# Kernel optimization log

Measured on AMD Instinct MI355X. Metric: run time of the kernel, lower is better.

The kernel has to match this reference:

```python
import jax, jax.numpy as jnp
import numpy as np

NODES = 23   # 22 players + ball per frame-graph
K = 8        # random neighbors per node
B, T = 64, 128
G = B * T            # total graphs (frames)
N = G * NODES        # total nodes
D_IN, H, RH = 16, 128, 128


def setup_inputs() -> dict:
    key = jax.random.key(0)
    ks = jax.random.split(key, 10)
    x = jax.random.normal(ks[0], (N, D_IN), jnp.float32)
    # per-graph random edges: dst = each node repeated K times, src = random node in same graph
    src_local = jax.random.randint(ks[1], (G, NODES * K), 0, NODES)
    dst_local = jnp.tile(jnp.repeat(jnp.arange(NODES), K)[None, :], (G, 1))
    off = (jnp.arange(G) * NODES)[:, None]
    edge_index = jnp.stack([(src_local + off).reshape(-1),
                            (dst_local + off).reshape(-1)]).astype(jnp.int32)
    runner_idx = jax.random.randint(ks[2], (G,), 0, NODES, dtype=jnp.int32)
    sc = lambda k, sh: (jax.random.normal(k, sh, jnp.float32) * 0.05)
    return {
        'x': x, 'edge_index': edge_index, 'runner_idx': runner_idx,
        'W1': sc(ks[3], (D_IN, H)), 'b1': jnp.zeros((H,), jnp.float32),
        'W2': sc(ks[4], (H, H)),    'b2': jnp.zeros((H,), jnp.float32),
        'W_ih': sc(ks[5], (3 * RH, H)), 'W_hh': sc(ks[6], (3 * RH, RH)),
        'b_ih': jnp.zeros((3 * RH,), jnp.float32), 'b_hh': jnp.zeros((3 * RH,), jnp.float32),
        'Wp': sc(ks[7], (RH, 2)), 'bp': jnp.zeros((2,), jnp.float32),
    }


def _gcn_conv(h, edge_index, W, b):
    # PyG GCNConv: add self-loops, symmetric normalization, scatter-sum
    h = h @ W
    loop = jnp.arange(N, dtype=edge_index.dtype)
    s = jnp.concatenate([edge_index[0], loop])
    d = jnp.concatenate([edge_index[1], loop])
    deg = jax.ops.segment_sum(jnp.ones_like(s, h.dtype), d, num_segments=N)
    dinv = jnp.where(deg > 0, jax.lax.rsqrt(deg), 0.0)
    norm = dinv[s] * dinv[d]                      # [E+N]
    out = jax.ops.segment_sum(h[s] * norm[:, None], d, num_segments=N)
    return out + b


def _gru(seq, W_ih, W_hh, b_ih, b_hh):
    # torch GRU: gates in r,z,n order
    xg = seq @ W_ih.T + b_ih                      # [B,T,3RH]
    def step(hprev, xt):
        gh = hprev @ W_hh.T + b_hh
        xr, xz, xn = jnp.split(xt, 3, axis=-1)
        hr, hz, hn = jnp.split(gh, 3, axis=-1)
        r = jax.nn.sigmoid(xr + hr)
        z = jax.nn.sigmoid(xz + hz)
        n = jnp.tanh(xn + r * hn)
        hnew = (1.0 - z) * n + z * hprev
        return hnew, hnew
    h0 = jnp.zeros((seq.shape[0], RH), seq.dtype)
    _, outs = jax.lax.scan(step, h0, jnp.swapaxes(xg, 0, 1))
    return jnp.swapaxes(outs, 0, 1)               # [B,T,RH]


def reference(x, edge_index, runner_idx, W1, b1, W2, b2,
              W_ih, W_hh, b_ih, b_hh, Wp, bp):
    h = jax.nn.relu(_gcn_conv(x, edge_index, W1, b1))
    h = jax.nn.relu(_gcn_conv(h, edge_index, W2, b2))
    # fused equivalent of the per-graph nonzero()/indexing loop:
    runner_global = jnp.arange(G, dtype=jnp.int32) * NODES + runner_idx
    seq = h[runner_global].reshape(B, T, H)       # all lengths == T, padding is a no-op
    out = _gru(seq, W_ih, W_hh, b_ih, b_hh)
    return out @ Wp + bp                          # [B,T,2]
```

## Files before the change

### kernel.cpp

```cpp
#include <hip/hip_runtime.h>
#include <hip/hip_bf16.h>
#include <math.h>

#define GG 8192
#define NODESN 23
#define KK 8
#define DIN 16
#define HH 128
#define RHH 128
#define EPG (NODESN*KK)
#define TTT 128
#define BBB 64

__global__ __launch_bounds__(256) void gcn_hsum(
    const float* __restrict__ x, const int* __restrict__ esrc,
    const int* __restrict__ runner,
    const float* __restrict__ W1, const float* __restrict__ b1,
    float* __restrict__ hsum_g)
{
    __shared__ float xs[NODESN * DIN];
    __shared__ int   srcs[EPG];
    __shared__ float t1[NODESN * HH];
    __shared__ float red[256];

    const int g   = blockIdx.x;
    const int tid = threadIdx.x;
    const int j   = tid & 127;
    const int nh  = tid >> 7;

    for (int i = tid; i < NODESN * DIN; i += 256) xs[i] = x[g * NODESN * DIN + i];
    for (int i = tid; i < EPG; i += 256)          srcs[i] = esrc[g * EPG + i] - g * NODESN;

    float w[DIN];
    #pragma unroll
    for (int k = 0; k < DIN; k++) w[k] = W1[k * HH + j];
    const float b1j = b1[j];
    __syncthreads();

    const int n0 = nh * 12;
    const int n1 = nh ? NODESN : 12;
    for (int n = n0; n < n1; n++) {
        float acc = 0.f;
        #pragma unroll
        for (int k = 0; k < DIN; k += 4) {
            float4 xv = *(const float4*)&xs[n * DIN + k];
            acc = fmaf(xv.x, w[k], fmaf(xv.y, w[k+1], fmaf(xv.z, w[k+2], fmaf(xv.w, w[k+3], acc))));
        }
        t1[n * HH + j] = acc;
    }
    __syncthreads();

    const int r = runner[g];
    float part = 0.f;
    for (int slot = nh; slot < 9; slot += 2) {
        int node = (slot < 8) ? srcs[r * KK + slot] : r;
        float acc = t1[node * HH + j];
        #pragma unroll
        for (int k = 0; k < KK; k++) acc += t1[srcs[node * KK + k] * HH + j];
        part += fmaxf(acc * (1.f / 9.f) + b1j, 0.f);
    }
    red[tid] = part;
    __syncthreads();
    if (tid < HH) hsum_g[(size_t)g * HH + tid] = red[tid] + red[tid + 128];
}

__global__ __launch_bounds__(256) void seq_kernel(
    const float* __restrict__ hsum_g, const float* __restrict__ W2,
    const float* __restrict__ b2, float* __restrict__ seq)
{
    __shared__ float hs[16 * HH];
    const int tid = threadIdx.x;
    const int j = tid & 127, mh = tid >> 7;
    const size_t base = (size_t)blockIdx.x * 16 * HH;

    for (int v = tid; v < 16 * HH / 4; v += 256)
        ((float4*)hs)[v] = ((const float4*)(hsum_g + base))[v];
    __syncthreads();

    float acc[8];
    #pragma unroll
    for (int m = 0; m < 8; m++) acc[m] = 0.f;
    const float* hrow = hs + mh * 8 * HH;
    for (int k = 0; k < HH; k += 4) {
        float w0  = W2[(k+0)*HH + j];
        float w1  = W2[(k+1)*HH + j];
        float w2v = W2[(k+2)*HH + j];
        float w3  = W2[(k+3)*HH + j];
        #pragma unroll
        for (int m = 0; m < 8; m++) {
            float4 hv = *(const float4*)&hrow[m * HH + k];
            acc[m] = fmaf(hv.x, w0, fmaf(hv.y, w1, fmaf(hv.z, w2v, fmaf(hv.w, w3, acc[m]))));
        }
    }
    const float bj = b2[j];
    #pragma unroll
    for (int m = 0; m < 8; m++)
        seq[base + (size_t)(mh * 8 + m) * HH + j] = fmaxf(acc[m] * (1.f/9.f) + bj, 0.f);
}

__global__ void transpose_wih(const float* __restrict__ W, float* __restrict__ WT)
{
    int idx = blockIdx.x * 256 + threadIdx.x;
    if (idx < 3 * RHH * RHH) {
        int jj = idx / RHH, kk = idx - jj * RHH;
        WT[kk * (3 * RHH) + jj] = W[idx];
    }
}

__global__ __launch_bounds__(384) void xg_kernel(
    const float* __restrict__ seq, const float* __restrict__ WT,
    const float* __restrict__ b_ih, float* __restrict__ xg)
{
    const int tid = threadIdx.x;
    const int m0 = blockIdx.x * 8;
    const float* srow = seq + (size_t)m0 * RHH;
    float acc[8];
    const float bv = b_ih[tid];
    #pragma unroll
    for (int mi = 0; mi < 8; mi++) acc[mi] = bv;
    for (int k = 0; k < RHH; k += 4) {
        float w0 = WT[(k+0)*384 + tid];
        float w1 = WT[(k+1)*384 + tid];
        float w2 = WT[(k+2)*384 + tid];
        float w3 = WT[(k+3)*384 + tid];
        #pragma unroll
        for (int mi = 0; mi < 8; mi++) {
            float4 sv = *(const float4*)(srow + mi * RHH + k);
            acc[mi] = fmaf(sv.x, w0, fmaf(sv.y, w1, fmaf(sv.z, w2, fmaf(sv.w, w3, acc[mi]))));
        }
    }
    #pragma unroll
    for (int mi = 0; mi < 8; mi++)
        xg[(size_t)(m0 + mi) * 384 + tid] = acc[mi];
}

#define CHUNK 64
#define XGBUF_FLOATS (CHUNK * 3 * RHH)
#define HOUT_FLOATS  (CHUNK * HH)

__global__ __launch_bounds__(1024)
__attribute__((amdgpu_waves_per_eu(4, 4)))
void gru_kernel(
    const float* __restrict__ xg, const float* __restrict__ W_hh,
    const float* __restrict__ b_hh, const float* __restrict__ Wp,
    const float* __restrict__ bp, float* __restrict__ out)
{
    __shared__ float xgbuf[XGBUF_FLOATS];
    __shared__ float houtb[HOUT_FLOATS];
    __shared__ float hpp[2 * HH];
    __shared__ float wps[2 * RHH + 2];

    const int b    = blockIdx.x;
    const int tid  = threadIdx.x;
    const int lane = tid & 63;
    const int q    = lane >> 3;
    const int i    = ((tid >> 6) << 3) | (lane & 7);

    float wr[16], wz[16], wn[16];
    int loff[4];
    {
        const float* br = W_hh + (size_t)i * RHH;
        const float* bz = br + (size_t)RHH * RHH;
        const float* bn = bz + (size_t)RHH * RHH;
        #pragma unroll
        for (int m = 0; m < 4; m++) {
            int p = (m + q) & 3;
            int o = q * 16 + 4 * p;
            loff[m] = o;
            float4 v;
            v = *(const float4*)(br + o); wr[4*m]=v.x; wr[4*m+1]=v.y; wr[4*m+2]=v.z; wr[4*m+3]=v.w;
            v = *(const float4*)(bz + o); wz[4*m]=v.x; wz[4*m+1]=v.y; wz[4*m+2]=v.z; wz[4*m+3]=v.w;
            v = *(const float4*)(bn + o); wn[4*m]=v.x; wn[4*m+1]=v.y; wn[4*m+2]=v.z; wn[4*m+3]=v.w;
        }
    }
    #pragma unroll
    for (int m = 0; m < 16; m++) {
        asm("" : "+v"(wr[m]));
        asm("" : "+v"(wz[m]));
        asm("" : "+v"(wn[m]));
    }

    const float bhr = b_hh[i];
    const float bhz = b_hh[RHH + i];
    const float bhn = b_hh[2 * RHH + i];

    if (tid < 2 * RHH) wps[tid] = Wp[tid];
    if (tid < 2)       wps[2 * RHH + tid] = bp[tid];
    if (tid < HH)      hpp[tid] = 0.f;
    float hprev = 0.f;

    const float* xbase = xg + (size_t)b * TTT * 3 * RHH;
    float* outb = out + (size_t)b * TTT * 2;

    for (int c = 0; c < TTT / CHUNK; c++) {
        {
            const float4* src = (const float4*)(xbase + (size_t)c * XGBUF_FLOATS);
            #pragma unroll
            for (int v = 0; v < XGBUF_FLOATS / 4 / 1024; v++)
                ((float4*)xgbuf)[tid + v * 1024] = src[tid + v * 1024];
        }
        if (c > 0) {
            const int s  = tid & 7;
            const int cc = (tid >> 3) & 1;
            const int tl = tid >> 4;
            const float* hr = &houtb[tl * HH + s * 16];
            float acc = 0.f;
            #pragma unroll
            for (int m = 0; m < 16; m += 4) {
                float4 hv = *(const float4*)(hr + m);
                int k = s * 16 + m;
                acc = fmaf(hv.x, wps[(k+0)*2 + cc],
                      fmaf(hv.y, wps[(k+1)*2 + cc],
                      fmaf(hv.z, wps[(k+2)*2 + cc],
                      fmaf(hv.w, wps[(k+3)*2 + cc], acc))));
            }
            acc += __shfl_xor(acc, 1); acc += __shfl_xor(acc, 2); acc += __shfl_xor(acc, 4);
            if (s == 0)
                outb[((c - 1) * CHUNK + tl) * 2 + cc] = acc + wps[2 * RHH + cc];
        }
        __syncthreads();

        for (int tl = 0; tl < CHUNK; tl++) {
            const float* hrow = &hpp[(tl & 1) * HH];
            float ar = 0.f, az = 0.f, an = 0.f;
            #pragma unroll
            for (int m = 0; m < 4; m++) {
                float4 hv = *(const float4*)(hrow + loff[m]);
                ar = fmaf(hv.x, wr[4*m], fmaf(hv.y, wr[4*m+1], fmaf(hv.z, wr[4*m+2], fmaf(hv.w, wr[4*m+3], ar))));
                az = fmaf(hv.x, wz[4*m], fmaf(hv.y, wz[4*m+1], fmaf(hv.z, wz[4*m+2], fmaf(hv.w, wz[4*m+3], az))));
                an = fmaf(hv.x, wn[4*m], fmaf(hv.y, wn[4*m+1], fmaf(hv.z, wn[4*m+2], fmaf(hv.w, wn[4*m+3], an))));
            }

            ar += __shfl_xor(ar, 8); ar += __shfl_xor(ar, 16); ar += __shfl_xor(ar, 32);
            az += __shfl_xor(az, 8); az += __shfl_xor(az, 16); az += __shfl_xor(az, 32);
            an += __shfl_xor(an, 8); an += __shfl_xor(an, 16); an += __shfl_xor(an, 32);

            {
                float xr = xgbuf[tl * 384 + i];
                float xz = xgbuf[tl * 384 + RHH + i];
                float xn = xgbuf[tl * 384 + 2 * RHH + i];
                float sr = xr + ar + bhr;
                float sz = xz + az + bhz;
                float rg = 1.f / (1.f + __expf(-sr));
                float zg = 1.f / (1.f + __expf(-sz));
                float tv = fmaf(rg, an + bhn, xn);
                tv = fminf(fmaxf(tv, -15.f), 15.f);
                float e2 = __expf(-2.f * tv);
                float ng = (1.f - e2) / (1.f + e2);
                hprev = fmaf(zg, hprev, (1.f - zg) * ng);
                if (q == 0) {
                    hpp[((tl + 1) & 1) * HH + i] = hprev;
                    houtb[tl * HH + i] = hprev;
                }
            }
            __syncthreads();
        }
    }

    {
        const int s  = tid & 7;
        const int cc = (tid >> 3) & 1;
        const int tl = tid >> 4;
        const float* hr = &houtb[tl * HH + s * 16];
        float acc = 0.f;
        #pragma unroll
        for (int m = 0; m < 16; m += 4) {
            float4 hv = *(const float4*)(hr + m);
            int k = s * 16 + m;
            acc = fmaf(hv.x, wps[(k+0)*2 + cc],
                  fmaf(hv.y, wps[(k+1)*2 + cc],
                  fmaf(hv.z, wps[(k+2)*2 + cc],
                  fmaf(hv.w, wps[(k+3)*2 + cc], acc))));
        }
        acc += __shfl_xor(acc, 1); acc += __shfl_xor(acc, 2); acc += __shfl_xor(acc, 4);
        if (s == 0)
            outb[((TTT / CHUNK - 1) * CHUNK + tl) * 2 + cc] = acc + wps[2 * RHH + cc];
    }
}

extern "C" void kernel_launch(void* const* d_in, const int* in_sizes, int n_in,
                              void* d_out, int out_size, void* d_ws, size_t ws_size,
                              hipStream_t stream)
{
    const float* x      = (const float*)d_in[0];
    const int*   eidx   = (const int*)d_in[1];
    const int*   runner = (const int*)d_in[2];
    const float* W1     = (const float*)d_in[3];
    const float* b1     = (const float*)d_in[4];
    const float* W2     = (const float*)d_in[5];
    const float* b2     = (const float*)d_in[6];
    const float* W_ih   = (const float*)d_in[7];
    const float* W_hh   = (const float*)d_in[8];
    const float* b_ih   = (const float*)d_in[9];
    const float* b_hh   = (const float*)d_in[10];
    const float* Wp     = (const float*)d_in[11];
    const float* bp     = (const float*)d_in[12];
    float* out = (float*)d_out;

    float* seq    = (float*)d_ws;
    float* xg     = seq + (size_t)GG * HH;
    float* WT     = xg + (size_t)GG * 3 * RHH;
    float* hsum_g = xg;

    transpose_wih<<<192, 256, 0, stream>>>(W_ih, WT);
    gcn_hsum<<<GG, 256, 0, stream>>>(x, eidx, runner, W1, b1, hsum_g);
    seq_kernel<<<GG / 16, 256, 0, stream>>>(hsum_g, W2, b2, seq);
    xg_kernel<<<GG / 8, 384, 0, stream>>>(seq, WT, b_ih, xg);
    gru_kernel<<<BBB, 1024, 0, stream>>>(xg, W_hh, b_hh, Wp, bp, out);
}
```

Before: 273.0 us.

## Remap GRU recurrence to 4 lanes per unit with DPP reductions

The GRU kernel now uses 512 threads where each hidden unit is computed by 4 lanes holding 32 weights per gate, instead of 8 lanes in a 1024-thread block. Cross-lane reductions use DPP row operations instead of shuffles. The xg chunk is repacked into an interleaved r/z/n float4 layout so each step does one LDS load. The previous-h ping-pong buffer is folded into the output history buffer. This targets per-step latency and barrier cost on the serial recurrence, at the price of more registers per thread and a strided gather for the xg load.

New measurement: 243.3 us. -10.9%, faster.

```diff
diff --git a/kernel.cpp b/kernel.cpp
--- a/kernel.cpp
+++ b/kernel.cpp
@@ -12,6 +12,15 @@
 #define TTT 128
 #define BBB 64
 
+template<int CTRL>
+static __device__ __forceinline__ float dpp_add(float v) {
+    int x = __builtin_amdgcn_update_dpp(0, __float_as_int(v), CTRL, 0xF, 0xF, true);
+    return v + __int_as_float(x);
+}
+#define DPP_XOR1 0xB1
+#define DPP_XOR2 0x4E
+#define DPP_SHL4 0x104
+
 __global__ __launch_bounds__(256) void gcn_hsum(
     const float* __restrict__ x, const int* __restrict__ esrc,
     const int* __restrict__ runner,
@@ -134,76 +143,67 @@
         xg[(size_t)(m0 + mi) * 384 + tid] = acc[mi];
 }
 
-#define CHUNK 64
-#define XGBUF_FLOATS (CHUNK * 3 * RHH)
-#define HOUT_FLOATS  (CHUNK * HH)
-
-__global__ __launch_bounds__(1024)
-__attribute__((amdgpu_waves_per_eu(4, 4)))
+#define CHUNK 32
+#define XGB_FLOATS (CHUNK * HH * 4)
+
+__global__ __launch_bounds__(512)
+__attribute__((amdgpu_waves_per_eu(2, 2)))
 void gru_kernel(
     const float* __restrict__ xg, const float* __restrict__ W_hh,
     const float* __restrict__ b_hh, const float* __restrict__ Wp,
     const float* __restrict__ bp, float* __restrict__ out)
 {
-    __shared__ float xgbuf[XGBUF_FLOATS];
-    __shared__ float houtb[HOUT_FLOATS];
-    __shared__ float hpp[2 * HH];
+    __shared__ float xgbuf[XGB_FLOATS];
+    __shared__ float houtb[(CHUNK + 2) * HH];
     __shared__ float wps[2 * RHH + 2];
 
-    const int b    = blockIdx.x;
-    const int tid  = threadIdx.x;
-    const int lane = tid & 63;
-    const int q    = lane >> 3;
-    const int i    = ((tid >> 6) << 3) | (lane & 7);
-
-    float wr[16], wz[16], wn[16];
-    int loff[4];
+    const int b   = blockIdx.x;
+    const int tid = threadIdx.x;
+    const int q   = tid & 3;
+    const int i   = tid >> 2;
+
+    float4 wrv[8], wzv[8], wnv[8];
+    int lof[8];
     {
-        const float* br = W_hh + (size_t)i * RHH;
+        const float* br = W_hh + (size_t)i * RHH + q * 32;
         const float* bz = br + (size_t)RHH * RHH;
         const float* bn = bz + (size_t)RHH * RHH;
         #pragma unroll
-        for (int m = 0; m < 4; m++) {
-            int p = (m + q) & 3;
-            int o = q * 16 + 4 * p;
-            loff[m] = o;
-            float4 v;
-            v = *(const float4*)(br + o); wr[4*m]=v.x; wr[4*m+1]=v.y; wr[4*m+2]=v.z; wr[4*m+3]=v.w;
-            v = *(const float4*)(bz + o); wz[4*m]=v.x; wz[4*m+1]=v.y; wz[4*m+2]=v.z; wz[4*m+3]=v.w;
-            v = *(const float4*)(bn + o); wn[4*m]=v.x; wn[4*m+1]=v.y; wn[4*m+2]=v.z; wn[4*m+3]=v.w;
-        }
-    }
-    #pragma unroll
-    for (int m = 0; m < 16; m++) {
-        asm("" : "+v"(wr[m]));
-        asm("" : "+v"(wz[m]));
-        asm("" : "+v"(wn[m]));
-    }
-
+        for (int m = 0; m < 8; m++) {
+            int p = (m + 2 * q) & 7;
+            lof[m] = q * 32 + 4 * p;
+            wrv[m] = *(const float4*)(br + 4 * p);
+            wzv[m] = *(const float4*)(bz + 4 * p);
+            wnv[m] = *(const float4*)(bn + 4 * p);
+        }
+    }
     const float bhr = b_hh[i];
     const float bhz = b_hh[RHH + i];
     const float bhn = b_hh[2 * RHH + i];
 
     if (tid < 2 * RHH) wps[tid] = Wp[tid];
     if (tid < 2)       wps[2 * RHH + tid] = bp[tid];
-    if (tid < HH)      hpp[tid] = 0.f;
+    if (tid < HH)      houtb[CHUNK * HH + tid] = 0.f;
     float hprev = 0.f;
 
     const float* xbase = xg + (size_t)b * TTT * 3 * RHH;
     float* outb = out + (size_t)b * TTT * 2;
 
     for (int c = 0; c < TTT / CHUNK; c++) {
-        {
-            const float4* src = (const float4*)(xbase + (size_t)c * XGBUF_FLOATS);
-            #pragma unroll
-            for (int v = 0; v < XGBUF_FLOATS / 4 / 1024; v++)
-                ((float4*)xgbuf)[tid + v * 1024] = src[tid + v * 1024];
+        #pragma unroll
+        for (int k2 = 0; k2 < 8; k2++) {
+            int slot = tid + (k2 << 9);
+            int tl = slot >> 7, ii = slot & 127;
+            const float* gsrc = xbase + (size_t)(c * CHUNK + tl) * 384 + ii;
+            float4 v;
+            v.x = gsrc[0]; v.y = gsrc[128]; v.z = gsrc[256]; v.w = 0.f;
+            *(float4*)&xgbuf[slot << 2] = v;
         }
         if (c > 0) {
             const int s  = tid & 7;
             const int cc = (tid >> 3) & 1;
             const int tl = tid >> 4;
-            const float* hr = &houtb[tl * HH + s * 16];
+            const float* hr = &houtb[(tl + 1) * HH + s * 16];
             float acc = 0.f;
             #pragma unroll
             for (int m = 0; m < 16; m += 4) {
@@ -214,45 +214,39 @@
                       fmaf(hv.z, wps[(k+2)*2 + cc],
                       fmaf(hv.w, wps[(k+3)*2 + cc], acc))));
             }
-            acc += __shfl_xor(acc, 1); acc += __shfl_xor(acc, 2); acc += __shfl_xor(acc, 4);
+            acc = dpp_add<DPP_XOR1>(acc);
+            acc = dpp_add<DPP_XOR2>(acc);
+            acc = dpp_add<DPP_SHL4>(acc);
             if (s == 0)
                 outb[((c - 1) * CHUNK + tl) * 2 + cc] = acc + wps[2 * RHH + cc];
         }
         __syncthreads();
 
         for (int tl = 0; tl < CHUNK; tl++) {
-            const float* hrow = &hpp[(tl & 1) * HH];
+            const float* hrow = &houtb[(tl == 0 ? CHUNK : tl) * HH];
+            float4 xgv = *(const float4*)&xgbuf[(tl * HH + i) << 2];
             float ar = 0.f, az = 0.f, an = 0.f;
             #pragma unroll
-            for (int m = 0; m < 4; m++) {
-                float4 hv = *(const float4*)(hrow + loff[m]);
-                ar = fmaf(hv.x, wr[4*m], fmaf(hv.y, wr[4*m+1], fmaf(hv.z, wr[4*m+2], fmaf(hv.w, wr[4*m+3], ar))));
-                az = fmaf(hv.x, wz[4*m], fmaf(hv.y, wz[4*m+1], fmaf(hv.z, wz[4*m+2], fmaf(hv.w, wz[4*m+3], az))));
-                an = fmaf(hv.x, wn[4*m], fmaf(hv.y, wn[4*m+1], fmaf(hv.z, wn[4*m+2], fmaf(hv.w, wn[4*m+3], an))));
+            for (int m = 0; m < 8; m++) {
+                float4 hv = *(const float4*)(hrow + lof[m]);
+                ar = fmaf(hv.x, wrv[m].x, fmaf(hv.y, wrv[m].y, fmaf(hv.z, wrv[m].z, fmaf(hv.w, wrv[m].w, ar))));
+                az = fmaf(hv.x, wzv[m].x, fmaf(hv.y, wzv[m].y, fmaf(hv.z, wzv[m].z, fmaf(hv.w, wzv[m].w, az))));
+                an = fmaf(hv.x, wnv[m].x, fmaf(hv.y, wnv[m].y, fmaf(hv.z, wnv[m].z, fmaf(hv.w, wnv[m].w, an))));
             }
-
-            ar += __shfl_xor(ar, 8); ar += __shfl_xor(ar, 16); ar += __shfl_xor(ar, 32);
-            az += __shfl_xor(az, 8); az += __shfl_xor(az, 16); az += __shfl_xor(az, 32);
-            an += __shfl_xor(an, 8); an += __shfl_xor(an, 16); an += __shfl_xor(an, 32);
-
-            {
-                float xr = xgbuf[tl * 384 + i];
-                float xz = xgbuf[tl * 384 + RHH + i];
-                float xn = xgbuf[tl * 384 + 2 * RHH + i];
-                float sr = xr + ar + bhr;
-                float sz = xz + az + bhz;
-                float rg = 1.f / (1.f + __expf(-sr));
-                float zg = 1.f / (1.f + __expf(-sz));
-                float tv = fmaf(rg, an + bhn, xn);
-                tv = fminf(fmaxf(tv, -15.f), 15.f);
-                float e2 = __expf(-2.f * tv);
-                float ng = (1.f - e2) / (1.f + e2);
-                hprev = fmaf(zg, hprev, (1.f - zg) * ng);
-                if (q == 0) {
-                    hpp[((tl + 1) & 1) * HH + i] = hprev;
-                    houtb[tl * HH + i] = hprev;
-                }
-            }
+            ar = dpp_add<DPP_XOR1>(ar); ar = dpp_add<DPP_XOR2>(ar);
+            az = dpp_add<DPP_XOR1>(az); az = dpp_add<DPP_XOR2>(az);
+            an = dpp_add<DPP_XOR1>(an); an = dpp_add<DPP_XOR2>(an);
+
+            float sr = xgv.x + ar + bhr;
+            float sz = xgv.y + az + bhz;
+            float rg = 1.f / (1.f + __expf(-sr));
+            float zg = 1.f / (1.f + __expf(-sz));
+            float tv = fmaf(rg, an + bhn, xgv.z);
+            tv = fminf(fmaxf(tv, -15.f), 15.f);
+            float e2 = __expf(-2.f * tv);
+            float ng = (1.f - e2) / (1.f + e2);
+            hprev = fmaf(zg, hprev, (1.f - zg) * ng);
+            if (q == 0) houtb[(tl + 1) * HH + i] = hprev;
             __syncthreads();
         }
     }
@@ -261,7 +255,7 @@
         const int s  = tid & 7;
         const int cc = (tid >> 3) & 1;
         const int tl = tid >> 4;
-        const float* hr = &houtb[tl * HH + s * 16];
+        const float* hr = &houtb[(tl + 1) * HH + s * 16];
         float acc = 0.f;
         #pragma unroll
         for (int m = 0; m < 16; m += 4) {
@@ -272,7 +266,9 @@
                   fmaf(hv.z, wps[(k+2)*2 + cc],
                   fmaf(hv.w, wps[(k+3)*2 + cc], acc))));
         }
-        acc += __shfl_xor(acc, 1); acc += __shfl_xor(acc, 2); acc += __shfl_xor(acc, 4);
+        acc = dpp_add<DPP_XOR1>(acc);
+        acc = dpp_add<DPP_XOR2>(acc);
+        acc = dpp_add<DPP_SHL4>(acc);
         if (s == 0)
             outb[((TTT / CHUNK - 1) * CHUNK + tl) * 2 + cc] = acc + wps[2 * RHH + cc];
     }
@@ -306,5 +302,5 @@
     gcn_hsum<<<GG, 256, 0, stream>>>(x, eidx, runner, W1, b1, hsum_g);
     seq_kernel<<<GG / 16, 256, 0, stream>>>(hsum_g, W2, b2, seq);
     xg_kernel<<<GG / 8, 384, 0, stream>>>(seq, WT, b_ih, xg);
-    gru_kernel<<<BBB, 1024, 0, stream>>>(xg, W_hh, b_hh, Wp, bp, out);
-}
+    gru_kernel<<<BBB, 512, 0, stream>>>(xg, W_hh, b_hh, Wp, bp, out);
+}
```
